# Kernel optimization log

Hardware: AMD Instinct MI355X
Metric: run time of the kernel (lower is better)

## Reference

```python
import math
import jax, jax.numpy as jnp
import numpy as np

TWO_PI = 2.0 * math.pi
EPS = 1e-6

F_DELTA, F_THETA, F_GAMMA = 2.0, 6.0, 40.0  # hard-coded band frequencies (Hz)
K_COUPLING = 2.0
N_STEPS = 10
DT = 0.01


def setup_inputs() -> dict:
    key = jax.random.key(0)
    ks = jax.random.split(key, 4)
    B, D = 32768, 2048
    nd, nt, ng = 32, 128, 512

    def xavier(k, fan_out, fan_in, gain=0.5):
        lim = gain * math.sqrt(6.0 / (fan_in + fan_out))
        return jax.random.uniform(k, (fan_out, fan_in), jnp.float32, -lim, lim)

    return {
        "x": jax.random.normal(ks[0], (B, D), jnp.float32),
        "W_delta": xavier(ks[1], nd, D),
        "W_theta": xavier(ks[2], nt, D),
        "W_gamma": xavier(ks[3], ng, D),
        "pac_depth_dt": jnp.float32(0.3),
        "pac_depth_tg": jnp.float32(0.3),
    }


def _mean_field(phase):
    # Kuramoto order parameter components, per batch row. phase: (B, n)
    C = jnp.mean(jnp.cos(phase), axis=-1, keepdims=True)
    S = jnp.mean(jnp.sin(phase), axis=-1, keepdims=True)
    return C, S


def _dynamics(dp, da, tp, ta, gp, ga, pac_dt, pac_tg):
    """Batched 3-band Kuramoto integration with cross-frequency PAC.

    Phases evolve under mean-field Kuramoto coupling within each band;
    the slow band's mean phase amplitude-modulates the next-faster band
    (delta->theta via pac_dt, theta->gamma via pac_tg). Euler, N_STEPS x DT.
    """
    def step(carry, _):
        dp, da, tp, ta, gp, ga = carry
        Cd, Sd = _mean_field(dp)
        Ct, St = _mean_field(tp)
        Cg, Sg = _mean_field(gp)
        # K * r * sin(psi - phi) == K * (S*cos(phi) - C*sin(phi))
        dp_n = (dp + DT * (TWO_PI * F_DELTA + K_COUPLING * (Sd * jnp.cos(dp) - Cd * jnp.sin(dp)))) % TWO_PI
        tp_n = (tp + DT * (TWO_PI * F_THETA + K_COUPLING * (St * jnp.cos(tp) - Ct * jnp.sin(tp)))) % TWO_PI
        gp_n = (gp + DT * (TWO_PI * F_GAMMA + K_COUPLING * (Sg * jnp.cos(gp) - Cg * jnp.sin(gp)))) % TWO_PI
        rd = jnp.sqrt(Cd * Cd + Sd * Sd) + EPS
        rt = jnp.sqrt(Ct * Ct + St * St) + EPS
        ta_n = jnp.maximum(ta * (1.0 + DT * pac_dt * (Cd / rd)), EPS)
        ga_n = jnp.maximum(ga * (1.0 + DT * pac_tg * (Ct / rt)), EPS)
        return (dp_n, da, tp_n, ta_n, gp_n, ga_n), None

    (dp, da, tp, ta, gp, ga), _ = jax.lax.scan(step, (dp, da, tp, ta, gp, ga), None, length=N_STEPS)
    return dp, da, tp, ta, gp, ga


def reference(x, W_delta, W_theta, W_gamma, pac_depth_dt, pac_depth_tg):
    # Three small dense projections define initial phases and amplitudes.
    zd = x @ W_delta.T  # (B, n_delta)
    zt = x @ W_theta.T  # (B, n_theta)
    zg = x @ W_gamma.T  # (B, n_gamma)
    da, ta, ga = (jnp.maximum(jnp.abs(z), EPS) for z in (zd, zt, zg))
    dp, tp, gp = (z % TWO_PI for z in (zd, zt, zg))
    # pac depths are detached in the torch module (.item()) before dynamics
    pac_dt = jax.lax.stop_gradient(jnp.clip(pac_depth_dt, 0.0, 1.0))
    pac_tg = jax.lax.stop_gradient(jnp.clip(pac_depth_tg, 0.0, 1.0))
    _, da, _, ta, _, ga = _dynamics(dp, da, tp, ta, gp, ga, pac_dt, pac_tg)
    return jnp.concatenate([da, ta, ga], axis=-1)  # (B, n_total)
```

## Files before the change

### kernel.cpp

```cpp
#include <hip/hip_runtime.h>
#include <stdint.h>

#define TWO_PI_F 6.28318530717958647692f
#define INV_2PI_F 0.15915494309189535f
#define EPSF 1e-6f
#define DTF 0.01f
#define KCOUP 2.0f
#define CPL (DTF * KCOUP * INV_2PI_F)

#define BM 128
#define BN 224
#define KITERS 64
#define NTILES 3
#define GTHREADS 256
#define B_TILE_BYTES 14336
#define A_TILE_BYTES 16384
#define W_IMG_BYTES ((size_t)KITERS * NTILES * B_TILE_BYTES)
#define WS_NEED W_IMG_BYTES

typedef __attribute__((ext_vector_type(8)))  __bf16         bf16x8;
typedef __attribute__((ext_vector_type(8)))  unsigned short ushort8v;
typedef __attribute__((ext_vector_type(16))) float          f32x16;

__device__ __forceinline__ unsigned short f2bf(float f) {
  unsigned u = __builtin_bit_cast(unsigned, f);
  u = (u + 0x7FFFu + ((u >> 16) & 1u)) >> 16;
  return (unsigned short)u;
}

__device__ __forceinline__ unsigned cvtpk(float lo, float hi) {
  unsigned r;
  asm("v_cvt_pk_bf16_f32 %0, %1, %2" : "=v"(r) : "v"(lo), "v"(hi));
  return r;
}

__global__ void prep_w(const float* __restrict__ Wd, const float* __restrict__ Wt,
                       const float* __restrict__ Wg, char* __restrict__ wbB) {
  int id = blockIdx.x * 256 + threadIdx.x;
  if (id >= 672 * 64) return;
  int col = id >> 6, t = id & 63;
  const float* src = (col < 32)  ? Wd + (size_t)col * 2048
                   : (col < 160) ? Wt + (size_t)(col - 32) * 2048
                                 : Wg + (size_t)(col - 160) * 2048;
  src += t * 32;
  const int n = col / BN, cin = col - n * BN;
  const int r = cin >> 1, par = cin & 1;
  char* dst = wbB + ((size_t)t * NTILES + n) * B_TILE_BYTES + r * 128;
  #pragma unroll
  for (int ls = 0; ls < 4; ls++) {
    float4 a = ((const float4*)src)[ls * 2];
    float4 b = ((const float4*)src)[ls * 2 + 1];
    ushort8v v;
    v[0] = f2bf(a.x); v[1] = f2bf(a.y); v[2] = f2bf(a.z); v[3] = f2bf(a.w);
    v[4] = f2bf(b.x); v[5] = f2bf(b.y); v[6] = f2bf(b.z); v[7] = f2bf(b.w);
    int p = (4 * par + ls) ^ (r & 7);
    *(ushort8v*)(dst + p * 16) = v;
  }
}

__launch_bounds__(GTHREADS, 3)
__global__ void gemm(const float* __restrict__ x, const char* __restrict__ wbB,
                     float* __restrict__ z) {
  __shared__ __align__(16) char smem[B_TILE_BYTES + A_TILE_BYTES];
  char* Bs = smem;
  char* As = smem + B_TILE_BYTES;

  const int tid = threadIdx.x;
  const int wid = tid >> 6, lane = tid & 63;
  const int cl = lane & 31, hk = lane >> 5;

  const int bid = blockIdx.x;
  const int xcd = bid & 7, j = bid >> 3;
  const int panel = xcd * 32 + j / NTILES;
  const int n = j % NTILES;
  const size_t row0 = (size_t)panel * BM;

  f32x16 acc[7];
  #pragma unroll
  for (int f = 0; f < 7; f++)
    #pragma unroll
    for (int jj = 0; jj < 16; jj++) acc[f][jj] = 0.f;

  const int arow_s = tid >> 3;
  const int aslot_log = (tid & 7) ^ (arow_s & 7);
  const float* asrc0 = x + (row0 + arow_s) * 2048 + aslot_log * 4;

  const int arf = wid * 32 + cl;
  const float* afbase = (const float*)(As + arf * 128);
  const int arf7 = arf & 7;

  const char* bimg = wbB + (size_t)n * B_TILE_BYTES;

  for (int t = 0; t < KITERS; t++) {
    __syncthreads();
    {
      const char* bsrc = bimg + (size_t)t * (NTILES * B_TILE_BYTES);
      #pragma unroll
      for (int rnd = 0; rnd < 3; rnd++) {
        int off = rnd * 4096 + tid * 16;
        __builtin_amdgcn_global_load_lds(
            (const __attribute__((address_space(1))) void*)(bsrc + off),
            (__attribute__((address_space(3))) void*)(Bs + off), 16, 0, 0);
      }
      if (tid < 128) {
        int off = 12288 + tid * 16;
        __builtin_amdgcn_global_load_lds(
            (const __attribute__((address_space(1))) void*)(bsrc + off),
            (__attribute__((address_space(3))) void*)(Bs + off), 16, 0, 0);
      }
      const float* asrc = asrc0 + t * 32;
      #pragma unroll
      for (int rnd = 0; rnd < 4; rnd++) {
        __builtin_amdgcn_global_load_lds(
            (const __attribute__((address_space(1))) void*)(asrc + (size_t)rnd * 32 * 2048),
            (__attribute__((address_space(3))) void*)(As + rnd * 4096 + tid * 16), 16, 0, 0);
      }
    }
    __syncthreads();
    #pragma unroll
    for (int s4 = 0; s4 < 2; s4++) {
      int ls = s4 * 4 + hk * 2;
      int p0 = ls ^ arf7;
      int p1 = p0 ^ 1;
      float4 lo = *(const float4*)(afbase + p0 * 4);
      float4 hi = *(const float4*)(afbase + p1 * 4);
      unsigned d0 = cvtpk(lo.x, lo.y), d1 = cvtpk(lo.z, lo.w);
      unsigned d2 = cvtpk(hi.x, hi.y), d3 = cvtpk(hi.z, hi.w);
      uint4 u = {d0, d1, d2, d3};
      bf16x8 af = __builtin_bit_cast(bf16x8, u);
      #pragma unroll
      for (int fn = 0; fn < 7; fn++) {
        int c = fn * 32 + cl;
        int r = c >> 1;
        int q = 4 * (c & 1) + s4 * 2 + hk;
        bf16x8 bfr = __builtin_bit_cast(bf16x8,
            *(const ushort8v*)(Bs + r * 128 + ((q ^ (r & 7)) << 4)));
        acc[fn] = __builtin_amdgcn_mfma_f32_32x32x16_bf16(af, bfr, acc[fn], 0, 0, 0);
      }
    }
  }

  #pragma unroll
  for (int fn = 0; fn < 7; fn++) {
    int col = n * BN + fn * 32 + cl;
    #pragma unroll
    for (int reg = 0; reg < 16; reg++) {
      int row = wid * 32 + (reg & 3) + ((reg >> 2) << 3) + (hk << 2);
      z[(row0 + row) * 672 + col] = acc[fn][reg];
    }
  }
}

__device__ __forceinline__ float wave_sum(float v) {
  v += __builtin_bit_cast(float, __builtin_amdgcn_update_dpp(
         0, __builtin_bit_cast(int, v), 0xB1, 0xF, 0xF, true));
  v += __builtin_bit_cast(float, __builtin_amdgcn_update_dpp(
         0, __builtin_bit_cast(int, v), 0x4E, 0xF, 0xF, true));
  v += __builtin_bit_cast(float, __builtin_amdgcn_update_dpp(
         0, __builtin_bit_cast(int, v), 0x141, 0xF, 0xF, true));
  v += __builtin_bit_cast(float, __builtin_amdgcn_update_dpp(
         0, __builtin_bit_cast(int, v), 0x140, 0xF, 0xF, true));
  v += __builtin_bit_cast(float, __builtin_amdgcn_ds_swizzle(
         __builtin_bit_cast(int, v), 0x401F));
  v += __shfl_xor(v, 32);
  return v;
}

#define ZSTR 164
#define DROWS 32
__launch_bounds__(256, 6)
__global__ void dyn_scale(float* __restrict__ z,
                          const float* __restrict__ pdt_p,
                          const float* __restrict__ ptg_p) {
  __shared__ float zdt[DROWS * ZSTR];
  __shared__ float Fbuf[2 * DROWS];
  const int tid = threadIdx.x;
  const int wid = tid >> 6, lane = tid & 63;
  const size_t row0 = (size_t)blockIdx.x * DROWS;

  for (int i = tid; i < DROWS * 40; i += 256) {
    int row = i / 40, c4 = i - row * 40;
    float4 v = *(const float4*)(z + (row0 + row) * 672 + c4 * 4);
    *(float4*)(&zdt[row * ZSTR + c4 * 4]) = v;
  }
  __syncthreads();

  const float pdt = fminf(fmaxf(pdt_p[0], 0.f), 1.f);
  const float ptg = fminf(fmaxf(ptg_p[0], 0.f), 1.f);

  for (int rr = 0; rr < 8; rr++) {
    int row = wid * 8 + rr;
    float pd  = ((lane < 32) ? zdt[row * ZSTR + lane] : 0.f) * INV_2PI_F;
    float pt0 = zdt[row * ZSTR + 32 + lane] * INV_2PI_F;
    float pt1 = zdt[row * ZSTR + 96 + lane] * INV_2PI_F;
    float Ft = 1.f, Fg = 1.f;
    for (int s = 0; s < 10; s++) {
      float qd = pd - floorf(pd), q0 = pt0 - floorf(pt0), q1 = pt1 - floorf(pt1);
      float sd, cd, s0, c0, s1, c1;
      asm("v_sin_f32 %0, %1" : "=v"(sd) : "v"(qd));
      asm("v_cos_f32 %0, %1" : "=v"(cd) : "v"(qd));
      asm("v_sin_f32 %0, %1" : "=v"(s0) : "v"(q0));
      asm("v_cos_f32 %0, %1" : "=v"(c0) : "v"(q0));
      asm("v_sin_f32 %0, %1" : "=v"(s1) : "v"(q1));
      asm("v_cos_f32 %0, %1" : "=v"(c1) : "v"(q1));
      float Cd = wave_sum((lane < 32) ? cd : 0.f) * (1.f / 32.f);
      float Sd = wave_sum((lane < 32) ? sd : 0.f) * (1.f / 32.f);
      float Ct = wave_sum(c0 + c1) * (1.f / 128.f);
      float St = wave_sum(s0 + s1) * (1.f / 128.f);
      pd  += DTF * 2.f + CPL * (Sd * cd - Cd * sd);
      pt0 += DTF * 6.f + CPL * (St * c0 - Ct * s0);
      pt1 += DTF * 6.f + CPL * (St * c1 - Ct * s1);
      float rdm = sqrtf(Cd * Cd + Sd * Sd) + EPSF;
      float rtm = sqrtf(Ct * Ct + St * St) + EPSF;
      Ft *= (1.f + DTF * pdt * (Cd / rdm));
      Fg *= (1.f + DTF * ptg * (Ct / rtm));
    }
    if (lane == 0) { Fbuf[row] = Ft; Fbuf[DROWS + row] = Fg; }
  }
  __syncthreads();

  for (int i = tid; i < DROWS * 168; i += 256) {
    int row = i / 168, c4 = i - row * 168;
    float4* p = (float4*)(z + (row0 + row) * 672 + c4 * 4);
    float4 v = (c4 < 40) ? *(const float4*)(&zdt[row * ZSTR + c4 * 4]) : *p;
    float f = (c4 < 8) ? 1.f : (c4 < 40 ? Fbuf[row] : Fbuf[DROWS + row]);
    v.x = fmaxf(fmaxf(fabsf(v.x), EPSF) * f, EPSF);
    v.y = fmaxf(fmaxf(fabsf(v.y), EPSF) * f, EPSF);
    v.z = fmaxf(fmaxf(fabsf(v.z), EPSF) * f, EPSF);
    v.w = fmaxf(fmaxf(fabsf(v.w), EPSF) * f, EPSF);
    *p = v;
  }
}

extern "C" void kernel_launch(void* const* d_in, const int* in_sizes, int n_in,
                              void* d_out, int out_size, void* d_ws, size_t ws_size,
                              hipStream_t stream) {
  const float* x   = (const float*)d_in[0];
  const float* Wd  = (const float*)d_in[1];
  const float* Wt  = (const float*)d_in[2];
  const float* Wg  = (const float*)d_in[3];
  const float* pdt = (const float*)d_in[4];
  const float* ptg = (const float*)d_in[5];
  float* outp = (float*)d_out;
  char* wbB = (char*)d_ws;

  if (ws_size < WS_NEED) return;

  const int Brows = in_sizes[0] / 2048;
  prep_w<<<(672 * 64 + 255) / 256, 256, 0, stream>>>(Wd, Wt, Wg, wbB);
  gemm<<<(Brows / BM) * NTILES, GTHREADS, 0, stream>>>(x, wbB, outp);
  dyn_scale<<<Brows / DROWS, 256, 0, stream>>>(outp, pdt, ptg);
}
```

Measured before the change: 223.5 us.

## Double-buffer LDS tiles to overlap global loads with MFMA compute

```diff
diff --git a/kernel.cpp b/kernel.cpp
--- a/kernel.cpp
+++ b/kernel.cpp
@@ -15,6 +15,7 @@
 #define GTHREADS 256
 #define B_TILE_BYTES 14336
 #define A_TILE_BYTES 16384
+#define BUF_BYTES (B_TILE_BYTES + A_TILE_BYTES)
 #define W_IMG_BYTES ((size_t)KITERS * NTILES * B_TILE_BYTES)
 #define WS_NEED W_IMG_BYTES
 
@@ -61,9 +62,7 @@
 __launch_bounds__(GTHREADS, 3)
 __global__ void gemm(const float* __restrict__ x, const char* __restrict__ wbB,
                      float* __restrict__ z) {
-  __shared__ __align__(16) char smem[B_TILE_BYTES + A_TILE_BYTES];
-  char* Bs = smem;
-  char* As = smem + B_TILE_BYTES;
+  __shared__ __align__(16) char smem[2 * BUF_BYTES];
 
   const int tid = threadIdx.x;
   const int wid = tid >> 6, lane = tid & 63;
@@ -86,59 +85,75 @@
   const float* asrc0 = x + (row0 + arow_s) * 2048 + aslot_log * 4;
 
   const int arf = wid * 32 + cl;
-  const float* afbase = (const float*)(As + arf * 128);
   const int arf7 = arf & 7;
 
   const char* bimg = wbB + (size_t)n * B_TILE_BYTES;
 
+#define STAGE(buf, t)                                                         \
+  { char* Bs_ = smem + (buf) * BUF_BYTES;                                     \
+    char* As_ = Bs_ + B_TILE_BYTES;                                           \
+    const char* bsrc = bimg + (size_t)(t) * (NTILES * B_TILE_BYTES);          \
+    _Pragma("unroll")                                                         \
+    for (int rnd = 0; rnd < 3; rnd++) {                                       \
+      int off = rnd * 4096 + tid * 16;                                        \
+      __builtin_amdgcn_global_load_lds(                                       \
+          (const __attribute__((address_space(1))) void*)(bsrc + off),        \
+          (__attribute__((address_space(3))) void*)(Bs_ + off), 16, 0, 0);    \
+    }                                                                         \
+    if (tid < 128) {                                                          \
+      int off = 12288 + tid * 16;                                             \
+      __builtin_amdgcn_global_load_lds(                                       \
+          (const __attribute__((address_space(1))) void*)(bsrc + off),        \
+          (__attribute__((address_space(3))) void*)(Bs_ + off), 16, 0, 0);    \
+    }                                                                         \
+    const float* asrc = asrc0 + (t) * 32;                                     \
+    _Pragma("unroll")                                                         \
+    for (int rnd = 0; rnd < 4; rnd++) {                                       \
+      __builtin_amdgcn_global_load_lds(                                       \
+          (const __attribute__((address_space(1))) void*)(asrc + (size_t)rnd * 32 * 2048), \
+          (__attribute__((address_space(3))) void*)(As_ + rnd * 4096 + tid * 16), 16, 0, 0); \
+    } }
+
+#define COMPUTE(buf)                                                          \
+  { const char* Bs_ = smem + (buf) * BUF_BYTES;                               \
+    const float* afb = (const float*)(Bs_ + B_TILE_BYTES + arf * 128);        \
+    _Pragma("unroll")                                                         \
+    for (int s4 = 0; s4 < 2; s4++) {                                          \
+      int ls = s4 * 4 + hk * 2;                                               \
+      int p0 = ls ^ arf7;                                                     \
+      int p1 = p0 ^ 1;                                                        \
+      float4 lo = *(const float4*)(afb + p0 * 4);                             \
+      float4 hi = *(const float4*)(afb + p1 * 4);                             \
+      unsigned d0 = cvtpk(lo.x, lo.y), d1 = cvtpk(lo.z, lo.w);                \
+      unsigned d2 = cvtpk(hi.x, hi.y), d3 = cvtpk(hi.z, hi.w);                \
+      uint4 u = {d0, d1, d2, d3};                                             \
+      bf16x8 af = __builtin_bit_cast(bf16x8, u);                              \
+      _Pragma("unroll")                                                       \
+      for (int fn = 0; fn < 7; fn++) {                                        \
+        int c = fn * 32 + cl;                                                 \
+        int r = c >> 1;                                                       \
+        int q = 4 * (c & 1) + s4 * 2 + hk;                                    \
+        bf16x8 bfr = __builtin_bit_cast(bf16x8,                               \
+            *(const ushort8v*)(Bs_ + r * 128 + ((q ^ (r & 7)) << 4)));        \
+        acc[fn] = __builtin_amdgcn_mfma_f32_32x32x16_bf16(af, bfr, acc[fn], 0, 0, 0); } } }
+
+  STAGE(0, 0);
   for (int t = 0; t < KITERS; t++) {
-    __syncthreads();
-    {
-      const char* bsrc = bimg + (size_t)t * (NTILES * B_TILE_BYTES);
-      #pragma unroll
-      for (int rnd = 0; rnd < 3; rnd++) {
-        int off = rnd * 4096 + tid * 16;
-        __builtin_amdgcn_global_load_lds(
-            (const __attribute__((address_space(1))) void*)(bsrc + off),
-            (__attribute__((address_space(3))) void*)(Bs + off), 16, 0, 0);
-      }
-      if (tid < 128) {
-        int off = 12288 + tid * 16;
-        __builtin_amdgcn_global_load_lds(
-            (const __attribute__((address_space(1))) void*)(bsrc + off),
-            (__attribute__((address_space(3))) void*)(Bs + off), 16, 0, 0);
-      }
-      const float* asrc = asrc0 + t * 32;
-      #pragma unroll
-      for (int rnd = 0; rnd < 4; rnd++) {
-        __builtin_amdgcn_global_load_lds(
-            (const __attribute__((address_space(1))) void*)(asrc + (size_t)rnd * 32 * 2048),
-            (__attribute__((address_space(3))) void*)(As + rnd * 4096 + tid * 16), 16, 0, 0);
-      }
+    const int cur = t & 1;
+    if (t + 1 < KITERS) {
+      STAGE(cur ^ 1, t + 1);
+      asm volatile("s_waitcnt vmcnt(7)" ::: "memory");
+    } else {
+      asm volatile("s_waitcnt vmcnt(0)" ::: "memory");
     }
-    __syncthreads();
-    #pragma unroll
-    for (int s4 = 0; s4 < 2; s4++) {
-      int ls = s4 * 4 + hk * 2;
-      int p0 = ls ^ arf7;
-      int p1 = p0 ^ 1;
-      float4 lo = *(const float4*)(afbase + p0 * 4);
-      float4 hi = *(const float4*)(afbase + p1 * 4);
-      unsigned d0 = cvtpk(lo.x, lo.y), d1 = cvtpk(lo.z, lo.w);
-      unsigned d2 = cvtpk(hi.x, hi.y), d3 = cvtpk(hi.z, hi.w);
-      uint4 u = {d0, d1, d2, d3};
-      bf16x8 af = __builtin_bit_cast(bf16x8, u);
-      #pragma unroll
-      for (int fn = 0; fn < 7; fn++) {
-        int c = fn * 32 + cl;
-        int r = c >> 1;
-        int q = 4 * (c & 1) + s4 * 2 + hk;
-        bf16x8 bfr = __builtin_bit_cast(bf16x8,
-            *(const ushort8v*)(Bs + r * 128 + ((q ^ (r & 7)) << 4)));
-        acc[fn] = __builtin_amdgcn_mfma_f32_32x32x16_bf16(af, bfr, acc[fn], 0, 0, 0);
-      }
-    }
-  }
+    __builtin_amdgcn_s_barrier();
+    __builtin_amdgcn_sched_barrier(0);
+    COMPUTE(cur);
+    __builtin_amdgcn_sched_barrier(0);
+    __builtin_amdgcn_s_barrier();
+  }
+#undef STAGE
+#undef COMPUTE
 
   #pragma unroll
   for (int fn = 0; fn < 7; fn++) {
```

New measurement: 287.8 us. 28.8% more time.
